# Kernel tuning notes

Hardware: AMD Instinct MI355X
Metric: run time of the kernel (lower is better)

The kernel has to match this reference:

```python
import jax, jax.numpy as jnp
import numpy as np

# Quantum layer math: each qubit starts in |0>, gets RX(x_i) then RY(theta_i),
#   <Z_i> = cos(x_i) * cos(theta_i)
# (RX rotates z->cos(x); RY then scales the z-component by cos(theta)).

def setup_inputs() -> dict:
    key = jax.random.key(0)
    k1, k2, k3, k4 = jax.random.split(key, 4)
    B, S, E, F = 32, 4096, 128, 512  # embed_dim == n_qubits == 128
    x = jax.random.normal(k1, (B, S, E), dtype=jnp.float32)
    theta = jax.random.normal(k2, (E,), dtype=jnp.float32)
    W1 = jax.random.normal(k3, (F, E), dtype=jnp.float32) * (1.0 / np.sqrt(E))
    W2 = jax.random.normal(k4, (E, F), dtype=jnp.float32) * (1.0 / np.sqrt(F))
    return {"x": x, "theta": theta, "W1": W1, "W2": W2}


def reference(x, theta, W1, W2):
    # Quantum expectation layer, fully vectorized over batch and sequence.
    q = jnp.cos(x) * jnp.cos(theta)  # [B, S, E]
    # Dropout is identity at inference. linear1 (no bias) -> relu -> linear2 (no bias).
    h = jax.nn.relu(jnp.einsum('bse,fe->bsf', q, W1))  # [B, S, F]
    out = jnp.einsum('bsf,ef->bse', h, W2)             # [B, S, E]
    return out
```

## Files before the change

kernel.cpp:

```cpp
#include <hip/hip_runtime.h>
#include <stdint.h>

typedef __attribute__((ext_vector_type(8))) short short8;
typedef __attribute__((ext_vector_type(4))) float floatx4;
typedef __attribute__((ext_vector_type(16))) float floatx16;
typedef __attribute__((ext_vector_type(2))) unsigned int uintx2;
typedef unsigned short u16;
typedef unsigned int u32;

#define EDIM 128
#define FDIM 512
#define BM 64
#define FC 128
#define QSTR (EDIM + 8)
#define HSTR (FC + 8)

__device__ __forceinline__ u32 f2bf_rne(float f) {
    u32 u = __builtin_bit_cast(u32, f);
    return (u + 0x7fffu + ((u >> 16) & 1u)) >> 16;
}
__device__ __forceinline__ u32 pk2bf(float lo, float hi) {
    return f2bf_rne(lo) | (f2bf_rne(hi) << 16);
}

__global__ __launch_bounds__(256) void ffq_prep(const float* __restrict__ W1,
                                                const float* __restrict__ W2,
                                                u16* __restrict__ wb) {
    int g = blockIdx.x * 256 + threadIdx.x;
    int lane = g & 63;
    int kk = (g >> 6) & 7;
    int idx = (g >> 9) & 15;
    int l31 = lane & 31, h5 = lane >> 5;
    const float* src;
    if (g < 8192) {
        src = W1 + (idx * 32 + l31) * EDIM + kk * 16 + h5 * 8;
    } else {
        int gg = idx >> 2, c = idx & 3;
        src = W2 + (gg * 32 + l31) * FDIM + c * 128 + kk * 16 + h5 * 8;
    }
    float4 v0 = *reinterpret_cast<const float4*>(src);
    float4 v1 = *reinterpret_cast<const float4*>(src + 4);
    uint4 p;
    p.x = pk2bf(v0.x, v0.y);
    p.y = pk2bf(v0.z, v0.w);
    p.z = pk2bf(v1.x, v1.y);
    p.w = pk2bf(v1.z, v1.w);
    reinterpret_cast<uint4*>(wb)[g] = p;
}

__global__ __launch_bounds__(512, 6) void ffq_main(const float* __restrict__ x,
                                                   const float* __restrict__ theta,
                                                   const u16* __restrict__ wb,
                                                   float* __restrict__ out) {
    __shared__ u16 qs[BM * QSTR];
    __shared__ u16 hs[2][BM * HSTR];

    const int t = threadIdx.x;
    const int lane = t & 63;
    const int wv = t >> 6;
    const int l31 = lane & 31;
    const int h5 = lane >> 5;
    const int mg = wv & 1;
    const int gg = wv >> 1;

    {
        const float4* xin = reinterpret_cast<const float4*>(x) +
                            (size_t)blockIdx.x * (BM * EDIM / 4);
        const int et = (t & 31) * 4;
        float c0 = __cosf(theta[et + 0]);
        float c1 = __cosf(theta[et + 1]);
        float c2 = __cosf(theta[et + 2]);
        float c3 = __cosf(theta[et + 3]);
        #pragma unroll
        for (int r = 0; r < 4; ++r) {
            int i = t + 512 * r;
            int m = i >> 5;
            float4 v = xin[i];
            uintx2 p;
            p.x = pk2bf(__cosf(v.x) * c0, __cosf(v.y) * c1);
            p.y = pk2bf(__cosf(v.z) * c2, __cosf(v.w) * c3);
            *reinterpret_cast<uintx2*>(&qs[m * QSTR + et]) = p;
        }
    }
    __syncthreads();

    const u16* W1s = wb;
    const u16* W2s = wb + FDIM * EDIM;

    floatx16 acc2 = {0.f,0.f,0.f,0.f,0.f,0.f,0.f,0.f,
                     0.f,0.f,0.f,0.f,0.f,0.f,0.f,0.f};

    const u16* qp  = &qs[(mg * 32 + l31) * QSTR + h5 * 8];
    const u16* hp0 = &hs[0][(mg * 32 + l31) * HSTR + h5 * 8];
    const u16* hp1 = &hs[1][(mg * 32 + l31) * HSTR + h5 * 8];

    #pragma unroll
    for (int c = 0; c < 4; ++c) {
        u16* hb = hs[c & 1];

        floatx16 acc1 = {0.f,0.f,0.f,0.f,0.f,0.f,0.f,0.f,
                         0.f,0.f,0.f,0.f,0.f,0.f,0.f,0.f};
        const u16* w1p = W1s + (size_t)(c * 4 + gg) * 4096 + lane * 8;
        #pragma unroll
        for (int k = 0; k < 8; ++k) {
            short8 a = *reinterpret_cast<const short8*>(w1p + k * 512);
            short8 b = *reinterpret_cast<const short8*>(qp + k * 16);
            acc1 = __builtin_amdgcn_mfma_f32_32x32x16_bf16(a, b, acc1, 0, 0, 0);
        }

        const int hrow = (mg * 32 + l31) * HSTR;
        #pragma unroll
        for (int rq = 0; rq < 4; ++rq) {
            const int fl = gg * 32 + rq * 8 + h5 * 4;
            uintx2 p;
            p.x = pk2bf(fmaxf(acc1[rq * 4 + 0], 0.f), fmaxf(acc1[rq * 4 + 1], 0.f));
            p.y = pk2bf(fmaxf(acc1[rq * 4 + 2], 0.f), fmaxf(acc1[rq * 4 + 3], 0.f));
            *reinterpret_cast<uintx2*>(&hb[hrow + fl]) = p;
        }
        __syncthreads();

        const u16* w2p = W2s + (size_t)(gg * 4 + c) * 4096 + lane * 8;
        const u16* hp = (c & 1) ? hp1 : hp0;
        #pragma unroll
        for (int k = 0; k < 8; ++k) {
            short8 a = *reinterpret_cast<const short8*>(w2p + k * 512);
            short8 b = *reinterpret_cast<const short8*>(hp + k * 16);
            acc2 = __builtin_amdgcn_mfma_f32_32x32x16_bf16(a, b, acc2, 0, 0, 0);
        }
    }

    float* op = out + (size_t)blockIdx.x * BM * EDIM +
                (mg * 32 + l31) * EDIM + gg * 32 + h5 * 4;
    #pragma unroll
    for (int rq = 0; rq < 4; ++rq) {
        floatx4 v;
        v[0] = acc2[rq * 4 + 0];
        v[1] = acc2[rq * 4 + 1];
        v[2] = acc2[rq * 4 + 2];
        v[3] = acc2[rq * 4 + 3];
        *reinterpret_cast<floatx4*>(op + rq * 8) = v;
    }
}

extern "C" void kernel_launch(void* const* d_in, const int* in_sizes, int n_in,
                              void* d_out, int out_size, void* d_ws, size_t ws_size,
                              hipStream_t stream) {
    const float* x     = (const float*)d_in[0];
    const float* theta = (const float*)d_in[1];
    const float* W1    = (const float*)d_in[2];
    const float* W2    = (const float*)d_in[3];
    u16* wb    = (u16*)d_ws;
    float* out = (float*)d_out;

    ffq_prep<<<64, 256, 0, stream>>>(W1, W2, wb);
    ffq_main<<<2048, 512, 0, stream>>>(x, theta, wb, out);
}
```

Before: 153.0 us.

## Make each wave own 32 full rows, keeping hidden activations in registers

Each wavefront now computes a full 32-row tile through both GEMMs. It holds q fragments and the relu hidden chunk in registers and uses v_permlane32_swap to turn the MFMA output layout into the next B operand. This removes shared memory and all __syncthreads, and cos(theta) is computed once in the prep kernel. The cost is more register pressure (four 16-wide accumulators plus q fragments), lower occupancy (256 threads, 3 blocks), and every wave streaming all weights from global/L2 with no LDS sharing.

```diff
diff --git a/kernel.cpp b/kernel.cpp
--- a/kernel.cpp
+++ b/kernel.cpp
@@ -4,16 +4,12 @@
 typedef __attribute__((ext_vector_type(8))) short short8;
 typedef __attribute__((ext_vector_type(4))) float floatx4;
 typedef __attribute__((ext_vector_type(16))) float floatx16;
-typedef __attribute__((ext_vector_type(2))) unsigned int uintx2;
+typedef __attribute__((ext_vector_type(4))) unsigned int uintx4;
 typedef unsigned short u16;
 typedef unsigned int u32;
 
 #define EDIM 128
 #define FDIM 512
-#define BM 64
-#define FC 128
-#define QSTR (EDIM + 8)
-#define HSTR (FC + 8)
 
 __device__ __forceinline__ u32 f2bf_rne(float f) {
     u32 u = __builtin_bit_cast(u32, f);
@@ -22,15 +18,28 @@
 __device__ __forceinline__ u32 pk2bf(float lo, float hi) {
     return f2bf_rne(lo) | (f2bf_rne(hi) << 16);
 }
+__device__ __forceinline__ u32 cvtpk(float lo, float hi) {
+    u32 r;
+    asm("v_cvt_pk_bf16_f32 %0, %1, %2" : "=v"(r) : "v"(lo), "v"(hi));
+    return r;
+}
+__device__ __forceinline__ void plswap(u32& a, u32& b) {
+    asm("v_permlane32_swap_b32 %0, %1" : "+v"(a), "+v"(b));
+}
 
 __global__ __launch_bounds__(256) void ffq_prep(const float* __restrict__ W1,
                                                 const float* __restrict__ W2,
+                                                const float* __restrict__ theta,
                                                 u16* __restrict__ wb) {
     int g = blockIdx.x * 256 + threadIdx.x;
     int lane = g & 63;
     int kk = (g >> 6) & 7;
     int idx = (g >> 9) & 15;
     int l31 = lane & 31, h5 = lane >> 5;
+    if (g < 128) {
+        float* cth = reinterpret_cast<float*>(wb + 2 * FDIM * EDIM);
+        cth[g] = cosf(theta[g]);
+    }
     const float* src;
     if (g < 8192) {
         src = W1 + (idx * 32 + l31) * EDIM + kk * 16 + h5 * 8;
@@ -48,97 +57,94 @@
     reinterpret_cast<uint4*>(wb)[g] = p;
 }
 
-__global__ __launch_bounds__(512, 6) void ffq_main(const float* __restrict__ x,
-                                                   const float* __restrict__ theta,
+__global__ __launch_bounds__(256, 3) void ffq_main(const float* __restrict__ x,
                                                    const u16* __restrict__ wb,
                                                    float* __restrict__ out) {
-    __shared__ u16 qs[BM * QSTR];
-    __shared__ u16 hs[2][BM * HSTR];
-
     const int t = threadIdx.x;
     const int lane = t & 63;
-    const int wv = t >> 6;
     const int l31 = lane & 31;
     const int h5 = lane >> 5;
-    const int mg = wv & 1;
-    const int gg = wv >> 1;
-
-    {
-        const float4* xin = reinterpret_cast<const float4*>(x) +
-                            (size_t)blockIdx.x * (BM * EDIM / 4);
-        const int et = (t & 31) * 4;
-        float c0 = __cosf(theta[et + 0]);
-        float c1 = __cosf(theta[et + 1]);
-        float c2 = __cosf(theta[et + 2]);
-        float c3 = __cosf(theta[et + 3]);
-        #pragma unroll
-        for (int r = 0; r < 4; ++r) {
-            int i = t + 512 * r;
-            int m = i >> 5;
-            float4 v = xin[i];
-            uintx2 p;
-            p.x = pk2bf(__cosf(v.x) * c0, __cosf(v.y) * c1);
-            p.y = pk2bf(__cosf(v.z) * c2, __cosf(v.w) * c3);
-            *reinterpret_cast<uintx2*>(&qs[m * QSTR + et]) = p;
-        }
-    }
-    __syncthreads();
+    const int gw = blockIdx.x * 4 + (t >> 6);
+    const size_t row0 = (size_t)gw * 32;
 
     const u16* W1s = wb;
     const u16* W2s = wb + FDIM * EDIM;
+    const float* cth = reinterpret_cast<const float*>(wb + 2 * FDIM * EDIM);
 
-    floatx16 acc2 = {0.f,0.f,0.f,0.f,0.f,0.f,0.f,0.f,
-                     0.f,0.f,0.f,0.f,0.f,0.f,0.f,0.f};
-
-    const u16* qp  = &qs[(mg * 32 + l31) * QSTR + h5 * 8];
-    const u16* hp0 = &hs[0][(mg * 32 + l31) * HSTR + h5 * 8];
-    const u16* hp1 = &hs[1][(mg * 32 + l31) * HSTR + h5 * 8];
-
-    #pragma unroll
-    for (int c = 0; c < 4; ++c) {
-        u16* hb = hs[c & 1];
-
-        floatx16 acc1 = {0.f,0.f,0.f,0.f,0.f,0.f,0.f,0.f,
-                         0.f,0.f,0.f,0.f,0.f,0.f,0.f,0.f};
-        const u16* w1p = W1s + (size_t)(c * 4 + gg) * 4096 + lane * 8;
+    short8 qf[8];
+    {
+        const float* xr = x + (row0 + l31) * EDIM + h5 * 8;
+        const float* tr = cth + h5 * 8;
         #pragma unroll
         for (int k = 0; k < 8; ++k) {
-            short8 a = *reinterpret_cast<const short8*>(w1p + k * 512);
-            short8 b = *reinterpret_cast<const short8*>(qp + k * 16);
-            acc1 = __builtin_amdgcn_mfma_f32_32x32x16_bf16(a, b, acc1, 0, 0, 0);
-        }
-
-        const int hrow = (mg * 32 + l31) * HSTR;
-        #pragma unroll
-        for (int rq = 0; rq < 4; ++rq) {
-            const int fl = gg * 32 + rq * 8 + h5 * 4;
-            uintx2 p;
-            p.x = pk2bf(fmaxf(acc1[rq * 4 + 0], 0.f), fmaxf(acc1[rq * 4 + 1], 0.f));
-            p.y = pk2bf(fmaxf(acc1[rq * 4 + 2], 0.f), fmaxf(acc1[rq * 4 + 3], 0.f));
-            *reinterpret_cast<uintx2*>(&hb[hrow + fl]) = p;
-        }
-        __syncthreads();
-
-        const u16* w2p = W2s + (size_t)(gg * 4 + c) * 4096 + lane * 8;
-        const u16* hp = (c & 1) ? hp1 : hp0;
-        #pragma unroll
-        for (int k = 0; k < 8; ++k) {
-            short8 a = *reinterpret_cast<const short8*>(w2p + k * 512);
-            short8 b = *reinterpret_cast<const short8*>(hp + k * 16);
-            acc2 = __builtin_amdgcn_mfma_f32_32x32x16_bf16(a, b, acc2, 0, 0, 0);
+            float4 x0 = *reinterpret_cast<const float4*>(xr + k * 16);
+            float4 x1 = *reinterpret_cast<const float4*>(xr + k * 16 + 4);
+            float4 t0 = *reinterpret_cast<const float4*>(tr + k * 16);
+            float4 t1 = *reinterpret_cast<const float4*>(tr + k * 16 + 4);
+            uintx4 u;
+            u[0] = cvtpk(__cosf(x0.x) * t0.x, __cosf(x0.y) * t0.y);
+            u[1] = cvtpk(__cosf(x0.z) * t0.z, __cosf(x0.w) * t0.w);
+            u[2] = cvtpk(__cosf(x1.x) * t1.x, __cosf(x1.y) * t1.y);
+            u[3] = cvtpk(__cosf(x1.z) * t1.z, __cosf(x1.w) * t1.w);
+            qf[k] = __builtin_bit_cast(short8, u);
         }
     }
 
-    float* op = out + (size_t)blockIdx.x * BM * EDIM +
-                (mg * 32 + l31) * EDIM + gg * 32 + h5 * 4;
+    const floatx16 zero = {0.f,0.f,0.f,0.f,0.f,0.f,0.f,0.f,
+                           0.f,0.f,0.f,0.f,0.f,0.f,0.f,0.f};
+    floatx16 acc[4] = {zero, zero, zero, zero};
+
+    const u16* w1l = W1s + lane * 8;
+    const u16* w2l = W2s + lane * 8;
+
+    for (int c = 0; c < 4; ++c) {
+        #pragma unroll
+        for (int f4 = 0; f4 < 4; ++f4) {
+            floatx16 a1 = zero;
+            const u16* w1p = w1l + (c * 4 + f4) * 4096;
+            #pragma unroll
+            for (int k = 0; k < 8; ++k) {
+                short8 a = *reinterpret_cast<const short8*>(w1p + k * 512);
+                a1 = __builtin_amdgcn_mfma_f32_32x32x16_bf16(a, qf[k], a1, 0, 0, 0);
+            }
+            u32 w[8];
+            #pragma unroll
+            for (int q = 0; q < 4; ++q) {
+                w[2*q]   = cvtpk(fmaxf(a1[4*q+0], 0.f), fmaxf(a1[4*q+1], 0.f));
+                w[2*q+1] = cvtpk(fmaxf(a1[4*q+2], 0.f), fmaxf(a1[4*q+3], 0.f));
+            }
+            plswap(w[0], w[2]);
+            plswap(w[1], w[3]);
+            plswap(w[4], w[6]);
+            plswap(w[5], w[7]);
+            uintx4 u0, u1;
+            u0[0] = w[0]; u0[1] = w[1]; u0[2] = w[2]; u0[3] = w[3];
+            u1[0] = w[4]; u1[1] = w[5]; u1[2] = w[6]; u1[3] = w[7];
+            short8 hb0 = __builtin_bit_cast(short8, u0);
+            short8 hb1 = __builtin_bit_cast(short8, u1);
+            #pragma unroll
+            for (int et = 0; et < 4; ++et) {
+                const u16* w2p = w2l + (et * 4 + c) * 4096 + f4 * 1024;
+                short8 b0 = *reinterpret_cast<const short8*>(w2p);
+                acc[et] = __builtin_amdgcn_mfma_f32_32x32x16_bf16(b0, hb0, acc[et], 0, 0, 0);
+                short8 b1 = *reinterpret_cast<const short8*>(w2p + 512);
+                acc[et] = __builtin_amdgcn_mfma_f32_32x32x16_bf16(b1, hb1, acc[et], 0, 0, 0);
+            }
+        }
+    }
+
+    float* op = out + (row0 + l31) * EDIM + h5 * 4;
     #pragma unroll
-    for (int rq = 0; rq < 4; ++rq) {
-        floatx4 v;
-        v[0] = acc2[rq * 4 + 0];
-        v[1] = acc2[rq * 4 + 1];
-        v[2] = acc2[rq * 4 + 2];
-        v[3] = acc2[rq * 4 + 3];
-        *reinterpret_cast<floatx4*>(op + rq * 8) = v;
+    for (int et = 0; et < 4; ++et) {
+        #pragma unroll
+        for (int rq = 0; rq < 4; ++rq) {
+            floatx4 v;
+            v[0] = acc[et][rq * 4 + 0];
+            v[1] = acc[et][rq * 4 + 1];
+            v[2] = acc[et][rq * 4 + 2];
+            v[3] = acc[et][rq * 4 + 3];
+            *reinterpret_cast<floatx4*>(op + et * 32 + rq * 8) = v;
+        }
     }
 }
 
@@ -152,6 +158,6 @@
     u16* wb    = (u16*)d_ws;
     float* out = (float*)d_out;
 
-    ffq_prep<<<64, 256, 0, stream>>>(W1, W2, wb);
-    ffq_main<<<2048, 512, 0, stream>>>(x, theta, wb, out);
+    ffq_prep<<<64, 256, 0, stream>>>(W1, W2, theta, wb);
+    ffq_main<<<1024, 256, 0, stream>>>(x, wb, out);
 }
```

Measured after the change: 240.2 us. +57.0%, slower.

## Make main kernel persistent with register prefetch of next x tile

Applied to the files above, without the earlier changes.

The main kernel becomes persistent: 512 blocks each loop over several 64-row tiles. While computing the current tile, each block loads the next tile's x into registers, so global-load latency overlaps with MFMA work. cos(theta) is computed once in the prep kernel and stored in the workspace. The q fragments are held in registers across the F-chunks, and the relu output is packed to bf16 with the hardware v_cvt_pk_bf16_f32 instruction instead of manual rounding. The trade-offs are fewer resident blocks, which limits latency hiding across blocks, and higher register pressure.

```diff
diff --git a/kernel.cpp b/kernel.cpp
--- a/kernel.cpp
+++ b/kernel.cpp
@@ -11,9 +11,10 @@
 #define EDIM 128
 #define FDIM 512
 #define BM 64
-#define FC 128
 #define QSTR (EDIM + 8)
-#define HSTR (FC + 8)
+#define HSTR (128 + 8)
+#define NTILE 2048
+#define GRID 512
 
 __device__ __forceinline__ u32 f2bf_rne(float f) {
     u32 u = __builtin_bit_cast(u32, f);
@@ -22,15 +23,25 @@
 __device__ __forceinline__ u32 pk2bf(float lo, float hi) {
     return f2bf_rne(lo) | (f2bf_rne(hi) << 16);
 }
+__device__ __forceinline__ u32 cvtpk(float lo, float hi) {
+    u32 r;
+    asm("v_cvt_pk_bf16_f32 %0, %1, %2" : "=v"(r) : "v"(lo), "v"(hi));
+    return r;
+}
 
 __global__ __launch_bounds__(256) void ffq_prep(const float* __restrict__ W1,
                                                 const float* __restrict__ W2,
+                                                const float* __restrict__ theta,
                                                 u16* __restrict__ wb) {
     int g = blockIdx.x * 256 + threadIdx.x;
     int lane = g & 63;
     int kk = (g >> 6) & 7;
     int idx = (g >> 9) & 15;
     int l31 = lane & 31, h5 = lane >> 5;
+    if (g < 128) {
+        float* cth = reinterpret_cast<float*>(wb + 2 * FDIM * EDIM);
+        cth[g] = cosf(theta[g]);
+    }
     const float* src;
     if (g < 8192) {
         src = W1 + (idx * 32 + l31) * EDIM + kk * 16 + h5 * 8;
@@ -48,8 +59,7 @@
     reinterpret_cast<uint4*>(wb)[g] = p;
 }
 
-__global__ __launch_bounds__(512, 6) void ffq_main(const float* __restrict__ x,
-                                                   const float* __restrict__ theta,
+__global__ __launch_bounds__(512, 4) void ffq_main(const float* __restrict__ x,
                                                    const u16* __restrict__ wb,
                                                    float* __restrict__ out) {
     __shared__ u16 qs[BM * QSTR];
@@ -63,82 +73,99 @@
     const int mg = wv & 1;
     const int gg = wv >> 1;
 
+    const u16* W1s = wb;
+    const u16* W2s = wb + FDIM * EDIM;
+    const float* cth = reinterpret_cast<const float*>(wb + 2 * FDIM * EDIM);
+
+    const int et = (t & 31) * 4;
+    const float c0 = cth[et + 0];
+    const float c1 = cth[et + 1];
+    const float c2 = cth[et + 2];
+    const float c3 = cth[et + 3];
+
+    const u16* w1l = W1s + lane * 8;
+    const u16* w2l = W2s + lane * 8;
+    const u16* qp  = &qs[(mg * 32 + l31) * QSTR + h5 * 8];
+
+    float4 xv[4];
     {
         const float4* xin = reinterpret_cast<const float4*>(x) +
                             (size_t)blockIdx.x * (BM * EDIM / 4);
-        const int et = (t & 31) * 4;
-        float c0 = __cosf(theta[et + 0]);
-        float c1 = __cosf(theta[et + 1]);
-        float c2 = __cosf(theta[et + 2]);
-        float c3 = __cosf(theta[et + 3]);
+        #pragma unroll
+        for (int r = 0; r < 4; ++r) xv[r] = xin[t + 512 * r];
+    }
+
+    for (int tile = blockIdx.x; tile < NTILE; tile += GRID) {
         #pragma unroll
         for (int r = 0; r < 4; ++r) {
-            int i = t + 512 * r;
-            int m = i >> 5;
-            float4 v = xin[i];
+            int m = (t + 512 * r) >> 5;
+            float4 v = xv[r];
             uintx2 p;
             p.x = pk2bf(__cosf(v.x) * c0, __cosf(v.y) * c1);
             p.y = pk2bf(__cosf(v.z) * c2, __cosf(v.w) * c3);
             *reinterpret_cast<uintx2*>(&qs[m * QSTR + et]) = p;
         }
-    }
-    __syncthreads();
+        __syncthreads();
 
-    const u16* W1s = wb;
-    const u16* W2s = wb + FDIM * EDIM;
-
-    floatx16 acc2 = {0.f,0.f,0.f,0.f,0.f,0.f,0.f,0.f,
-                     0.f,0.f,0.f,0.f,0.f,0.f,0.f,0.f};
-
-    const u16* qp  = &qs[(mg * 32 + l31) * QSTR + h5 * 8];
-    const u16* hp0 = &hs[0][(mg * 32 + l31) * HSTR + h5 * 8];
-    const u16* hp1 = &hs[1][(mg * 32 + l31) * HSTR + h5 * 8];
-
-    #pragma unroll
-    for (int c = 0; c < 4; ++c) {
-        u16* hb = hs[c & 1];
-
-        floatx16 acc1 = {0.f,0.f,0.f,0.f,0.f,0.f,0.f,0.f,
-                         0.f,0.f,0.f,0.f,0.f,0.f,0.f,0.f};
-        const u16* w1p = W1s + (size_t)(c * 4 + gg) * 4096 + lane * 8;
-        #pragma unroll
-        for (int k = 0; k < 8; ++k) {
-            short8 a = *reinterpret_cast<const short8*>(w1p + k * 512);
-            short8 b = *reinterpret_cast<const short8*>(qp + k * 16);
-            acc1 = __builtin_amdgcn_mfma_f32_32x32x16_bf16(a, b, acc1, 0, 0, 0);
+        if (tile + GRID < NTILE) {
+            const float4* xin = reinterpret_cast<const float4*>(x) +
+                                (size_t)(tile + GRID) * (BM * EDIM / 4);
+            #pragma unroll
+            for (int r = 0; r < 4; ++r) xv[r] = xin[t + 512 * r];
         }
 
-        const int hrow = (mg * 32 + l31) * HSTR;
+        short8 qf[8];
+        #pragma unroll
+        for (int k = 0; k < 8; ++k)
+            qf[k] = *reinterpret_cast<const short8*>(qp + k * 16);
+
+        floatx16 acc2 = {0.f,0.f,0.f,0.f,0.f,0.f,0.f,0.f,
+                         0.f,0.f,0.f,0.f,0.f,0.f,0.f,0.f};
+
+        #pragma unroll
+        for (int c = 0; c < 4; ++c) {
+            floatx16 acc1 = {0.f,0.f,0.f,0.f,0.f,0.f,0.f,0.f,
+                             0.f,0.f,0.f,0.f,0.f,0.f,0.f,0.f};
+            const u16* w1p = w1l + (size_t)(c * 4 + gg) * 4096;
+            #pragma unroll
+            for (int k = 0; k < 8; ++k) {
+                short8 a = *reinterpret_cast<const short8*>(w1p + k * 512);
+                acc1 = __builtin_amdgcn_mfma_f32_32x32x16_bf16(a, qf[k], acc1, 0, 0, 0);
+            }
+
+            u16* hb = hs[c & 1];
+            const int hrow = (mg * 32 + l31) * HSTR;
+            #pragma unroll
+            for (int rq = 0; rq < 4; ++rq) {
+                const int fl = gg * 32 + rq * 8 + h5 * 4;
+                uintx2 p;
+                p.x = cvtpk(fmaxf(acc1[rq * 4 + 0], 0.f), fmaxf(acc1[rq * 4 + 1], 0.f));
+                p.y = cvtpk(fmaxf(acc1[rq * 4 + 2], 0.f), fmaxf(acc1[rq * 4 + 3], 0.f));
+                *reinterpret_cast<uintx2*>(&hb[hrow + fl]) = p;
+            }
+            __syncthreads();
+
+            const u16* w2p = w2l + (size_t)(gg * 4 + c) * 4096;
+            const u16* hpc = &hs[c & 1][(mg * 32 + l31) * HSTR + h5 * 8];
+            #pragma unroll
+            for (int k = 0; k < 8; ++k) {
+                short8 a = *reinterpret_cast<const short8*>(w2p + k * 512);
+                short8 b = *reinterpret_cast<const short8*>(hpc + k * 16);
+                acc2 = __builtin_amdgcn_mfma_f32_32x32x16_bf16(a, b, acc2, 0, 0, 0);
+            }
+        }
+
+        float* op = out + (size_t)tile * BM * EDIM +
+                    (mg * 32 + l31) * EDIM + gg * 32 + h5 * 4;
         #pragma unroll
         for (int rq = 0; rq < 4; ++rq) {
-            const int fl = gg * 32 + rq * 8 + h5 * 4;
-            uintx2 p;
-            p.x = pk2bf(fmaxf(acc1[rq * 4 + 0], 0.f), fmaxf(acc1[rq * 4 + 1], 0.f));
-            p.y = pk2bf(fmaxf(acc1[rq * 4 + 2], 0.f), fmaxf(acc1[rq * 4 + 3], 0.f));
-            *reinterpret_cast<uintx2*>(&hb[hrow + fl]) = p;
+            floatx4 v;
+            v[0] = acc2[rq * 4 + 0];
+            v[1] = acc2[rq * 4 + 1];
+            v[2] = acc2[rq * 4 + 2];
+            v[3] = acc2[rq * 4 + 3];
+            *reinterpret_cast<floatx4*>(op + rq * 8) = v;
         }
-        __syncthreads();
-
-        const u16* w2p = W2s + (size_t)(gg * 4 + c) * 4096 + lane * 8;
-        const u16* hp = (c & 1) ? hp1 : hp0;
-        #pragma unroll
-        for (int k = 0; k < 8; ++k) {
-            short8 a = *reinterpret_cast<const short8*>(w2p + k * 512);
-            short8 b = *reinterpret_cast<const short8*>(hp + k * 16);
-            acc2 = __builtin_amdgcn_mfma_f32_32x32x16_bf16(a, b, acc2, 0, 0, 0);
-        }
-    }
-
-    float* op = out + (size_t)blockIdx.x * BM * EDIM +
-                (mg * 32 + l31) * EDIM + gg * 32 + h5 * 4;
-    #pragma unroll
-    for (int rq = 0; rq < 4; ++rq) {
-        floatx4 v;
-        v[0] = acc2[rq * 4 + 0];
-        v[1] = acc2[rq * 4 + 1];
-        v[2] = acc2[rq * 4 + 2];
-        v[3] = acc2[rq * 4 + 3];
-        *reinterpret_cast<floatx4*>(op + rq * 8) = v;
     }
 }
 
@@ -152,6 +179,6 @@
     u16* wb    = (u16*)d_ws;
     float* out = (float*)d_out;
 
-    ffq_prep<<<64, 256, 0, stream>>>(W1, W2, wb);
-    ffq_main<<<2048, 512, 0, stream>>>(x, theta, wb, out);
+    ffq_prep<<<64, 256, 0, stream>>>(W1, W2, theta, wb);
+    ffq_main<<<GRID, 512, 0, stream>>>(x, wb, out);
 }
```

Measured after the change: 270.6 us. +76.9%, slower.
